# Kernel optimization log

Measured on AMD Instinct MI355X. Metric: run time of the kernel, lower is better.

## Reference

```python
import jax, jax.numpy as jnp
import numpy as np

B, T, D, H = 4, 2048, 1024, 16
HD = D // H  # 64


def setup_inputs() -> dict:
    key = jax.random.key(0)
    ks = jax.random.split(key, 5)
    return {
        "x": jax.random.normal(ks[0], (B, T, D), dtype=jnp.float32),
        "W_qkv": jax.random.normal(ks[1], (D, 3 * D), dtype=jnp.float32) * 0.02,
        "b_qkv": jax.random.normal(ks[2], (3 * D,), dtype=jnp.float32) * 0.02,
        "W_out": jax.random.normal(ks[3], (D, D), dtype=jnp.float32) * 0.02,
        "b_out": jax.random.normal(ks[4], (D,), dtype=jnp.float32) * 0.02,
        "mask": 1,
    }


def reference(x, W_qkv, b_qkv, W_out, b_out, mask):
    # fused QKV projection: (B,T,3D)
    qkv = x @ W_qkv + b_qkv
    # torch layout: view (B,T,H,3*hd) then chunk last dim into q,k,v
    qkv = qkv.reshape(B, T, H, 3, HD)
    q = qkv[..., 0, :].transpose(0, 2, 1, 3)  # (B,H,T,hd)
    k = qkv[..., 1, :].transpose(0, 2, 1, 3)
    v = qkv[..., 2, :].transpose(0, 2, 1, 3)
    scores = jnp.einsum('bhqd,bhkd->bhqk', q, k) / jnp.sqrt(jnp.float32(HD))
    if mask:
        causal = jnp.triu(jnp.ones((T, T), dtype=bool), k=1)
        scores = jnp.where(causal[None, None], jnp.float32(-jnp.inf), scores)
    attn = jax.nn.softmax(scores, axis=-1)
    out = jnp.einsum('bhqk,bhkd->bhqd', attn, v)  # (B,H,T,hd)
    out = out.transpose(0, 2, 1, 3).reshape(B, T, D)
    return out @ W_out + b_out
```

## Files before the change

kernel.cpp:

```cpp
#include <hip/hip_runtime.h>

typedef unsigned short u16;
typedef __bf16 bf16x8 __attribute__((ext_vector_type(8)));
typedef float f32x4 __attribute__((ext_vector_type(4)));
typedef float f32x16 __attribute__((ext_vector_type(16)));

#define DEV __device__ __forceinline__

constexpr int Bb = 4, Tt = 2048, Dd = 1024, Hh = 16, HDd = 64;
constexpr int MM = Bb * Tt;
constexpr float QSCALE = 0.125f * 1.4426950408889634f;

DEV u16 f2bf(float f) {
  unsigned u = __float_as_uint(f);
  u += 0x7fffu + ((u >> 16) & 1u);
  return (u16)(u >> 16);
}

DEV unsigned cvtpk(float a, float b) {
  unsigned r;
  asm("v_cvt_pk_bf16_f32 %0, %1, %2" : "=v"(r) : "v"(a), "v"(b));
  return r;
}

DEV void pswap(unsigned& a, unsigned& b) {
  asm("v_permlane32_swap_b32 %0, %1" : "+v"(a), "+v"(b));
}

DEV void gload_lds16(const u16* g, u16* l) {
  __builtin_amdgcn_global_load_lds(
      (const __attribute__((address_space(1))) void*)g,
      (__attribute__((address_space(3))) void*)l, 16, 0, 0);
}

__global__ __launch_bounds__(256) void cast_x_kernel(const float* __restrict__ in,
                                                     u16* __restrict__ out, int n8) {
  int i = blockIdx.x * 256 + threadIdx.x;
  if (i >= n8) return;
  const float4* p = (const float4*)in + (size_t)i * 2;
  float4 v0 = p[0], v1 = p[1];
  union { u16 u[8]; uint4 v; } t;
  t.u[0] = f2bf(v0.x); t.u[1] = f2bf(v0.y); t.u[2] = f2bf(v0.z); t.u[3] = f2bf(v0.w);
  t.u[4] = f2bf(v1.x); t.u[5] = f2bf(v1.y); t.u[6] = f2bf(v1.z); t.u[7] = f2bf(v1.w);
  ((uint4*)out)[i] = t.v;
}

__global__ __launch_bounds__(256) void wcast_t_kernel(const float* __restrict__ in,
                                                      u16* __restrict__ out, int K, int N) {
  __shared__ float tile[32][33];
  int n0 = blockIdx.x * 32, k0 = blockIdx.y * 32;
  int tx = threadIdx.x & 31, ty = threadIdx.x >> 5;
  #pragma unroll
  for (int yy = ty; yy < 32; yy += 8)
    tile[yy][tx] = in[(size_t)(k0 + yy) * N + n0 + tx];
  __syncthreads();
  #pragma unroll
  for (int yy = ty; yy < 32; yy += 8)
    out[(size_t)(n0 + yy) * K + k0 + tx] = f2bf(tile[tx][yy]);
}

DEV void stageA128(const u16* __restrict__ src, int row0, int k0, int ld, u16* lds) {
  int t = threadIdx.x;
  int r = t >> 2, slot = t & 3;
  int c = (slot ^ ((r >> 1) & 3)) << 3;
  gload_lds16(src + (size_t)(row0 + r) * ld + k0 + c, lds + (size_t)(t & ~63) * 8);
}
DEV void stageB256(const u16* __restrict__ src, int row0, int k0, int ld, u16* lds) {
  int t = threadIdx.x;
  #pragma unroll
  for (int j = 0; j < 2; ++j) {
    int e = j * 512 + t;
    int r = e >> 2, slot = e & 3;
    int c = (slot ^ ((r >> 1) & 3)) << 3;
    gload_lds16(src + (size_t)(row0 + r) * ld + k0 + c,
                lds + (size_t)(j * 512 + (t & ~63)) * 8);
  }
}

__global__ __launch_bounds__(512, 4) void gemm_qkv_kernel(
    const u16* __restrict__ A, const u16* __restrict__ Bt,
    const float* __restrict__ bias,
    u16* __restrict__ Qb, u16* __restrict__ Kb, u16* __restrict__ Vtb,
    int M, int N, int Kd) {
  __shared__ __align__(16) u16 SH[36864];
  int nx = N >> 8;
  int bid = blockIdx.y * nx + blockIdx.x;
  int nwg = (M >> 7) * nx;
  int swz = (bid & 7) * (nwg >> 3) + (bid >> 3);
  int m0 = (swz / nx) * 128, n0 = (swz % nx) * 256;

  int tid = threadIdx.x, l = tid & 63, w = tid >> 6;
  int lo = l & 15, g = l >> 4;
  int wm = (w >> 2) * 64, wn = (w & 3) * 64;
  f32x4 acc[4][4] = {};
  int nk = Kd >> 5;
  stageA128(A, m0, 0, Kd, SH);
  stageB256(Bt, n0, 0, Kd, SH + 12288);
  stageA128(A, m0, 32, Kd, SH + 4096);
  stageB256(Bt, n0, 32, Kd, SH + 12288 + 8192);
  asm volatile("s_waitcnt vmcnt(3)" ::: "memory");
  __builtin_amdgcn_s_barrier();
  for (int kt = 0; kt < nk; ++kt) {
    if (kt + 2 < nk) {
      int bi = (kt + 2) % 3;
      stageA128(A, m0, (kt + 2) * 32, Kd, SH + bi * 4096);
      stageB256(Bt, n0, (kt + 2) * 32, Kd, SH + 12288 + bi * 8192);
    }
    const u16* Ac = SH + (kt % 3) * 4096;
    const u16* Bc = SH + 12288 + (kt % 3) * 8192;
    bf16x8 a[4], b[4];
    #pragma unroll
    for (int i = 0; i < 4; ++i) {
      int row = wm + i * 16 + lo;
      a[i] = *(const bf16x8*)&Ac[row * 32 + ((g ^ ((row >> 1) & 3)) << 3)];
    }
    #pragma unroll
    for (int j = 0; j < 4; ++j) {
      int row = wn + j * 16 + lo;
      b[j] = *(const bf16x8*)&Bc[row * 32 + ((g ^ ((row >> 1) & 3)) << 3)];
    }
    __builtin_amdgcn_s_setprio(1);
    #pragma unroll
    for (int i = 0; i < 4; ++i)
      #pragma unroll
      for (int j = 0; j < 4; ++j)
        acc[i][j] = __builtin_amdgcn_mfma_f32_16x16x32_bf16(a[i], b[j], acc[i][j], 0, 0, 0);
    __builtin_amdgcn_s_setprio(0);
    if (kt + 2 < nk) {
      asm volatile("s_waitcnt vmcnt(3)" ::: "memory");
    } else {
      asm volatile("s_waitcnt vmcnt(0)" ::: "memory");
    }
    __builtin_amdgcn_s_barrier();
  }
  #pragma unroll
  for (int round = 0; round < 2; ++round) {
    if ((w >> 2) == round) {
      u16* ep = SH + (w & 3) * 4096;
      int nblk = n0 + wn;
      int hh = nblk / 192, which = (nblk % 192) >> 6;
      int mblk = m0 + wm;
      int b_ = mblk >> 11, t0 = mblk & (Tt - 1);
      if (which == 2) {
        #pragma unroll
        for (int j = 0; j < 4; ++j) {
          float bv = bias[nblk + j * 16 + lo];
          int rowp = j * 16 + lo;
          #pragma unroll
          for (int i = 0; i < 4; ++i) {
            int slotp = i * 2 + (g >> 1);
            #pragma unroll
            for (int r = 0; r < 4; ++r) {
              ep[rowp * 64 + ((slotp ^ (rowp & 7)) << 3) + (g & 1) * 4 + r] =
                  f2bf(acc[i][j][r] + bv);
            }
          }
        }
        asm volatile("s_waitcnt lgkmcnt(0)" ::: "memory");
        u16* dst = Vtb + (size_t)(b_ * Hh + hh) * HDd * Tt + t0;
        #pragma unroll
        for (int s = 0; s < 8; ++s) {
          int row = s * 8 + (l >> 3);
          int phys = ((l & 7) ^ (row & 7)) << 3;
          uint4 v = *(const uint4*)&ep[row * 64 + phys];
          *(uint4*)(dst + (size_t)row * Tt + (l & 7) * 8) = v;
        }
      } else {
        float qs = (which == 0) ? QSCALE : 1.0f;
        #pragma unroll
        for (int j = 0; j < 4; ++j) {
          float bv = bias[nblk + j * 16 + lo];
          int slot = j * 2 + (lo >> 3);
          #pragma unroll
          for (int i = 0; i < 4; ++i) {
            #pragma unroll
            for (int r = 0; r < 4; ++r) {
              int lrow = i * 16 + g * 4 + r;
              ep[lrow * 64 + ((slot ^ (lrow & 7)) << 3) + (lo & 7)] =
                  f2bf((acc[i][j][r] + bv) * qs);
            }
          }
        }
        asm volatile("s_waitcnt lgkmcnt(0)" ::: "memory");
        u16* dst = (which == 0) ? Qb : Kb;
        dst += ((size_t)(b_ * Hh + hh) * Tt + t0) * HDd;
        #pragma unroll
        for (int s = 0; s < 8; ++s) {
          int row = s * 8 + (l >> 3);
          int phys = ((l & 7) ^ (row & 7)) << 3;
          uint4 v = *(const uint4*)&ep[row * 64 + phys];
          *(uint4*)(dst + row * 64 + (l & 7) * 8) = v;
        }
      }
    }
    __syncthreads();
  }
}

DEV void stage_tile(const u16* __restrict__ src, int row0, int k0, int ld, u16* lds) {
  int t = threadIdx.x, w = t >> 6;
  #pragma unroll
  for (int j = 0; j < 2; ++j) {
    int e = (j * 256 + t) * 8;
    int r = e >> 5;
    int slot = (e >> 3) & 3;
    int c = (slot ^ ((r >> 1) & 3)) << 3;
    gload_lds16(src + (size_t)(row0 + r) * ld + k0 + c, lds + j * 2048 + w * 512);
  }
}

__global__ __launch_bounds__(256) void gemm_out_kernel(
    const u16* __restrict__ A, const u16* __restrict__ Bt,
    const float* __restrict__ bias, float* __restrict__ Cf,
    int M, int N, int Kd) {
  __shared__ __align__(16) u16 SH[24576];
  int nx = N >> 7;
  int bid = blockIdx.y * nx + blockIdx.x;
  int nwg = (M >> 7) * nx;
  int swz = (bid & 7) * (nwg >> 3) + (bid >> 3);
  int m0 = (swz / nx) * 128, n0 = (swz % nx) * 128;

  int tid = threadIdx.x, l = tid & 63, w = tid >> 6;
  int lo = l & 15, g = l >> 4;
  int wm = (w >> 1) * 64, wn = (w & 1) * 64;
  f32x4 acc[4][4] = {};
  int nk = Kd >> 5;
  stage_tile(A, m0, 0, Kd, SH);
  stage_tile(Bt, n0, 0, Kd, SH + 12288);
  stage_tile(A, m0, 32, Kd, SH + 4096);
  stage_tile(Bt, n0, 32, Kd, SH + 12288 + 4096);
  asm volatile("s_waitcnt vmcnt(4)" ::: "memory");
  __builtin_amdgcn_s_barrier();
  for (int kt = 0; kt < nk; ++kt) {
    if (kt + 2 < nk) {
      int bi = (kt + 2) % 3;
      stage_tile(A, m0, (kt + 2) * 32, Kd, SH + bi * 4096);
      stage_tile(Bt, n0, (kt + 2) * 32, Kd, SH + 12288 + bi * 4096);
    }
    const u16* Ac = SH + (kt % 3) * 4096;
    const u16* Bc = SH + 12288 + (kt % 3) * 4096;
    bf16x8 a[4], b[4];
    #pragma unroll
    for (int i = 0; i < 4; ++i) {
      int row = wm + i * 16 + lo;
      a[i] = *(const bf16x8*)&Ac[row * 32 + ((g ^ ((row >> 1) & 3)) << 3)];
    }
    #pragma unroll
    for (int j = 0; j < 4; ++j) {
      int row = wn + j * 16 + lo;
      b[j] = *(const bf16x8*)&Bc[row * 32 + ((g ^ ((row >> 1) & 3)) << 3)];
    }
    #pragma unroll
    for (int i = 0; i < 4; ++i)
      #pragma unroll
      for (int j = 0; j < 4; ++j)
        acc[i][j] = __builtin_amdgcn_mfma_f32_16x16x32_bf16(a[i], b[j], acc[i][j], 0, 0, 0);
    if (kt + 2 < nk) {
      asm volatile("s_waitcnt vmcnt(4)" ::: "memory");
    } else {
      asm volatile("s_waitcnt vmcnt(0)" ::: "memory");
    }
    __builtin_amdgcn_s_barrier();
  }
  #pragma unroll
  for (int j = 0; j < 4; ++j) {
    int n = n0 + wn + j * 16 + lo;
    float bv = bias[n];
    #pragma unroll
    for (int i = 0; i < 4; ++i) {
      #pragma unroll
      for (int r = 0; r < 4; ++r) {
        int m = m0 + wm + i * 16 + g * 4 + r;
        Cf[(size_t)m * N + n] = acc[i][j][r] + bv;
      }
    }
  }
}

DEV void stage512(const u16* __restrict__ g, size_t rstride, u16* lds) {
  int t = threadIdx.x;
  int r = t >> 3, pp = t & 7;
  int lg = pp ^ (r & 7);
  gload_lds16(g + (size_t)r * rstride + lg * 8, lds + (size_t)(t & ~63) * 8);
}

DEV void build_pfrags(const f32x16& s, bf16x8& f0, bf16x8& f1) {
  unsigned w0 = cvtpk(s[0], s[1]),  w1 = cvtpk(s[2], s[3]);
  unsigned w2 = cvtpk(s[4], s[5]),  w3 = cvtpk(s[6], s[7]);
  unsigned w4 = cvtpk(s[8], s[9]),  w5 = cvtpk(s[10], s[11]);
  unsigned w6 = cvtpk(s[12], s[13]), w7 = cvtpk(s[14], s[15]);
  pswap(w0, w2);
  pswap(w1, w3);
  pswap(w4, w6);
  pswap(w5, w7);
  union { unsigned u[4]; bf16x8 v; } t0, t1;
  t0.u[0] = w0; t0.u[1] = w1; t0.u[2] = w2; t0.u[3] = w3;
  t1.u[0] = w4; t1.u[1] = w5; t1.u[2] = w6; t1.u[3] = w7;
  f0 = t0.v; f1 = t1.v;
}

DEV void write_o(u16* __restrict__ O, size_t rowbase, const f32x16& o0,
                 const f32x16& o1, float L, int hf) {
  float inv = 1.0f / L;
  #pragma unroll
  for (int m = 0; m < 4; ++m) {
    uint2 v0, v1;
    v0.x = cvtpk(o0[4 * m] * inv,     o0[4 * m + 1] * inv);
    v0.y = cvtpk(o0[4 * m + 2] * inv, o0[4 * m + 3] * inv);
    *(uint2*)(O + rowbase + m * 8 + hf * 4) = v0;
    v1.x = cvtpk(o1[4 * m] * inv,     o1[4 * m + 1] * inv);
    v1.y = cvtpk(o1[4 * m + 2] * inv, o1[4 * m + 3] * inv);
    *(uint2*)(O + rowbase + 32 + m * 8 + hf * 4) = v1;
  }
}

__global__ __launch_bounds__(512) void attn_kernel(const u16* __restrict__ Q,
                                                   const u16* __restrict__ K,
                                                   const u16* __restrict__ Vt,
                                                   u16* __restrict__ O) {
  __shared__ __align__(16) u16 Ks[4][4096];
  __shared__ __align__(16) u16 Vs[4][4096];
  __shared__ float MLs[8][64][2];
  __shared__ float OSs[4][64][8];
  int p = blockIdx.y & 7;
  int bh = ((int)blockIdx.y >> 3) * 8 + (int)blockIdx.x;
  int b_ = bh >> 4, h = bh & 15;
  const u16* Qp = Q + (size_t)bh * Tt * HDd;
  const u16* Kp = K + (size_t)bh * Tt * HDd;
  const u16* Vp = Vt + (size_t)bh * HDd * Tt;
  int tid = threadIdx.x, w = tid >> 6, l = tid & 63;
  int wq = w & 3, grp = w >> 2;
  int lq = l & 31, hf = l >> 5;
  int JA = 15 - p, JB = p;
  int ntA = 2 * JA + 2;
  constexpr int ntT = 34;

  int q0 = 128 * JA + 32 * wq;
  int qrow = q0 + lq;
  int swz = lq & 7;

  bf16x8 aq[4];
  #pragma unroll
  for (int s = 0; s < 4; ++s)
    aq[s] = *(const bf16x8*)(Qp + (size_t)qrow * HDd + s * 16 + hf * 8);

  f32x16 o0 = {}, o1 = {};
  float M = -1e30f, L = 0.f;

  stage512(Kp, HDd, Ks[0]);
  stage512(Vp, Tt, Vs[0]);
  stage512(Kp + (size_t)64 * HDd, HDd, Ks[1]);
  stage512(Vp + 64, Tt, Vs[1]);
  asm volatile("s_waitcnt vmcnt(0)" ::: "memory");
  __builtin_amdgcn_s_barrier();

  int jB = ntA >> 1;
  for (int j = 0; j < ntT / 2; ++j) {
    int t2 = 2 * j + 2;
    if (t2 < ntT) {
      int kt2 = (t2 < ntA ? t2 : t2 - ntA) * 64;
      stage512(Kp + (size_t)kt2 * HDd, HDd, Ks[t2 & 3]);
      stage512(Vp + kt2, Tt, Vs[t2 & 3]);
      int t3 = t2 + 1;
      int kt3 = (t3 < ntA ? t3 : t3 - ntA) * 64;
      stage512(Kp + (size_t)kt3 * HDd, HDd, Ks[t3 & 3]);
      stage512(Vp + kt3, Tt, Vs[t3 & 3]);
    }
    if (j == jB) {
      MLs[w][l][0] = M; MLs[w][l][1] = L;
      asm volatile("s_waitcnt lgkmcnt(0)" ::: "memory");
      __builtin_amdgcn_s_barrier();
      float Mb = MLs[w ^ 4][l][0], Lb = MLs[w ^ 4][l][1];
      float Mstar = fmaxf(M, Mb);
      float ss = __builtin_amdgcn_exp2f(M - Mstar);
      float sb = __builtin_amdgcn_exp2f(Mb - Mstar);
      float Lm = L * ss + Lb * sb;
      #pragma unroll
      for (int r = 0; r < 16; ++r) { o0[r] *= ss; o1[r] *= ss; }
      #pragma unroll
      for (int c = 0; c < 4; ++c) {
        if (w >= 4) {
          #pragma unroll
          for (int k = 0; k < 8; ++k)
            OSs[wq][l][k] = (c < 2) ? o0[(c & 1) * 8 + k] : o1[(c & 1) * 8 + k];
        }
        asm volatile("s_waitcnt lgkmcnt(0)" ::: "memory");
        __builtin_amdgcn_s_barrier();
        if (w < 4) {
          #pragma unroll
          for (int k = 0; k < 8; ++k) {
            float v = OSs[wq][l][k];
            if (c < 2) o0[(c & 1) * 8 + k] += v; else o1[(c & 1) * 8 + k] += v;
          }
        }
        asm volatile("s_waitcnt lgkmcnt(0)" ::: "memory");
        __builtin_amdgcn_s_barrier();
      }
      if (w < 4) {
        size_t rbA = ((size_t)b_ * Tt + qrow) * Dd + h * HDd;
        write_o(O, rbA, o0, o1, Lm, hf);
      }
      #pragma unroll
      for (int r = 0; r < 16; ++r) { o0[r] = 0.f; o1[r] = 0.f; }
      M = -1e30f; L = 0.f;
      q0 = 128 * JB + 32 * wq;
      qrow = q0 + lq;
      #pragma unroll
      for (int s = 0; s < 4; ++s)
        aq[s] = *(const bf16x8*)(Qp + (size_t)qrow * HDd + s * 16 + hf * 8);
    }
    int myt = 2 * j + grp;
    int kt = (myt < ntA ? myt : myt - ntA) * 64;
    const u16* Kc = Ks[myt & 3];
    const u16* Vc = Vs[myt & 3];
    if (kt < q0 + 32) {
      f32x16 s0 = {}, s1 = {};
      __builtin_amdgcn_s_setprio(1);
      #pragma unroll
      for (int ds = 0; ds < 4; ++ds) {
        int slot = 2 * ds + hf;
        bf16x8 k0 = *(const bf16x8*)&Kc[lq * 64 + ((slot ^ swz) << 3)];
        bf16x8 k1 = *(const bf16x8*)&Kc[(32 + lq) * 64 + ((slot ^ swz) << 3)];
        s0 = __builtin_amdgcn_mfma_f32_32x32x16_bf16(k0, aq[ds], s0, 0, 0, 0);
        s1 = __builtin_amdgcn_mfma_f32_32x32x16_bf16(k1, aq[ds], s1, 0, 0, 0);
      }
      __builtin_amdgcn_s_setprio(0);
      if (kt + 63 > q0) {
        #pragma unroll
        for (int r = 0; r < 16; ++r) {
          int kg = kt + (r & 3) + 8 * (r >> 2) + 4 * hf;
          if (kg > qrow)      s0[r] = -INFINITY;
          if (kg + 32 > qrow) s1[r] = -INFINITY;
        }
      }
      float mx_[16];
      #pragma unroll
      for (int r = 0; r < 16; ++r) mx_[r] = fmaxf(s0[r], s1[r]);
      #pragma unroll
      for (int st = 8; st >= 1; st >>= 1)
        #pragma unroll
        for (int r = 0; r < 16; ++r) if (r < st) mx_[r] = fmaxf(mx_[r], mx_[r + st]);
      float mx = fmaxf(mx_[0], __shfl_xor(mx_[0], 32));
      float sc = 1.f;
      if (!__all(mx <= M + 8.f)) {
        float Mn = fmaxf(M, mx);
        sc = __builtin_amdgcn_exp2f(M - Mn);
        M = Mn;
        #pragma unroll
        for (int r = 0; r < 16; ++r) { o0[r] *= sc; o1[r] *= sc; }
      }
      #pragma unroll
      for (int r = 0; r < 16; ++r) {
        s0[r] = __builtin_amdgcn_exp2f(s0[r] - M);
        s1[r] = __builtin_amdgcn_exp2f(s1[r] - M);
      }
      float ls_[16];
      #pragma unroll
      for (int r = 0; r < 16; ++r) ls_[r] = s0[r] + s1[r];
      #pragma unroll
      for (int st = 8; st >= 1; st >>= 1)
        #pragma unroll
        for (int r = 0; r < 16; ++r) if (r < st) ls_[r] += ls_[r + st];
      float ls = ls_[0] + __shfl_xor(ls_[0], 32);
      L = L * sc + ls;
      bf16x8 pf0, pf1, pf2, pf3;
      build_pfrags(s0, pf0, pf1);
      build_pfrags(s1, pf2, pf3);
      __builtin_amdgcn_s_setprio(1);
      #pragma unroll
      for (int ks = 0; ks < 4; ++ks) {
        int slot = 2 * ks + hf;
        bf16x8 v0 = *(const bf16x8*)&Vc[lq * 64 + ((slot ^ swz) << 3)];
        bf16x8 v1 = *(const bf16x8*)&Vc[(32 + lq) * 64 + ((slot ^ swz) << 3)];
        bf16x8 pf = (ks == 0) ? pf0 : (ks == 1) ? pf1 : (ks == 2) ? pf2 : pf3;
        o0 = __builtin_amdgcn_mfma_f32_32x32x16_bf16(v0, pf, o0, 0, 0, 0);
        o1 = __builtin_amdgcn_mfma_f32_32x32x16_bf16(v1, pf, o1, 0, 0, 0);
      }
      __builtin_amdgcn_s_setprio(0);
    }
    asm volatile("s_waitcnt vmcnt(0)" ::: "memory");
    __builtin_amdgcn_s_barrier();
  }

  MLs[w][l][0] = M; MLs[w][l][1] = L;
  asm volatile("s_waitcnt lgkmcnt(0)" ::: "memory");
  __builtin_amdgcn_s_barrier();
  float Mb = MLs[w ^ 4][l][0], Lb = MLs[w ^ 4][l][1];
  float Mstar = fmaxf(M, Mb);
  float ss = __builtin_amdgcn_exp2f(M - Mstar);
  float sb = __builtin_amdgcn_exp2f(Mb - Mstar);
  float Lm = L * ss + Lb * sb;
  #pragma unroll
  for (int r = 0; r < 16; ++r) { o0[r] *= ss; o1[r] *= ss; }
  #pragma unroll
  for (int c = 0; c < 4; ++c) {
    if (w >= 4) {
      #pragma unroll
      for (int k = 0; k < 8; ++k)
        OSs[wq][l][k] = (c < 2) ? o0[(c & 1) * 8 + k] : o1[(c & 1) * 8 + k];
    }
    asm volatile("s_waitcnt lgkmcnt(0)" ::: "memory");
    __builtin_amdgcn_s_barrier();
    if (w < 4) {
      #pragma unroll
      for (int k = 0; k < 8; ++k) {
        float v = OSs[wq][l][k];
        if (c < 2) o0[(c & 1) * 8 + k] += v; else o1[(c & 1) * 8 + k] += v;
      }
    }
    asm volatile("s_waitcnt lgkmcnt(0)" ::: "memory");
    __builtin_amdgcn_s_barrier();
  }
  if (w < 4) {
    size_t rbB = ((size_t)b_ * Tt + qrow) * Dd + h * HDd;
    write_o(O, rbB, o0, o1, Lm, hf);
  }
}

extern "C" void kernel_launch(void* const* d_in, const int* in_sizes, int n_in,
                              void* d_out, int out_size, void* d_ws, size_t ws_size,
                              hipStream_t stream) {
  const float* x    = (const float*)d_in[0];
  const float* Wqkv = (const float*)d_in[1];
  const float* bqkv = (const float*)d_in[2];
  const float* Wout = (const float*)d_in[3];
  const float* bout = (const float*)d_in[4];
  float* out = (float*)d_out;
  char* ws = (char*)d_ws;

  u16* xb    = (u16*)(ws + 0);
  u16* Ob    = (u16*)(ws + 0);
  u16* Wqkvt = (u16*)(ws + 16777216);
  u16* Woutt = (u16*)(ws + 23068672);
  u16* Qb    = (u16*)(ws + 25165824);
  u16* Kb    = (u16*)(ws + 41943040);
  u16* Vtb   = (u16*)(ws + 58720256);

  cast_x_kernel<<<4096, 256, 0, stream>>>(x, xb, (MM * Dd) / 8);
  wcast_t_kernel<<<dim3(96, 32), 256, 0, stream>>>(Wqkv, Wqkvt, Dd, 3 * Dd);
  wcast_t_kernel<<<dim3(32, 32), 256, 0, stream>>>(Wout, Woutt, Dd, Dd);
  gemm_qkv_kernel<<<dim3(12, 64), 512, 0, stream>>>(
      xb, Wqkvt, bqkv, Qb, Kb, Vtb, MM, 3 * Dd, Dd);
  attn_kernel<<<dim3(8, 64), 512, 0, stream>>>(Qb, Kb, Vtb, Ob);
  gemm_out_kernel<<<dim3(8, 64), 256, 0, stream>>>(
      Ob, Woutt, bout, out, MM, Dd, Dd);
}
```

Before: 172.4 us.

## Widen output GEMM to 128x256 tiles and split attention merge into smaller chunks

The output projection GEMM now uses 128x256 tiles with 512 threads (8 waves) instead of 128x128 with 256 threads. It reuses stageA128/stageB256 helpers that appear to exist elsewhere, and raises wave priority around the MFMA block. This is meant to improve reuse of the A operand and cut the number of workgroups, at the cost of more LDS per block. Separately, the attention kernel's cross-wave output merge now moves 4 floats per step over 8 barrier rounds instead of 8 floats over 4, which halves that LDS scratch but adds barriers.

```diff
diff --git a/kernel.cpp b/kernel.cpp
--- a/kernel.cpp
+++ b/kernel.cpp
@@ -197,48 +197,36 @@
   }
 }
 
-DEV void stage_tile(const u16* __restrict__ src, int row0, int k0, int ld, u16* lds) {
-  int t = threadIdx.x, w = t >> 6;
-  #pragma unroll
-  for (int j = 0; j < 2; ++j) {
-    int e = (j * 256 + t) * 8;
-    int r = e >> 5;
-    int slot = (e >> 3) & 3;
-    int c = (slot ^ ((r >> 1) & 3)) << 3;
-    gload_lds16(src + (size_t)(row0 + r) * ld + k0 + c, lds + j * 2048 + w * 512);
-  }
-}
-
-__global__ __launch_bounds__(256) void gemm_out_kernel(
+__global__ __launch_bounds__(512, 4) void gemm_out256_kernel(
     const u16* __restrict__ A, const u16* __restrict__ Bt,
     const float* __restrict__ bias, float* __restrict__ Cf,
     int M, int N, int Kd) {
-  __shared__ __align__(16) u16 SH[24576];
-  int nx = N >> 7;
+  __shared__ __align__(16) u16 SH[36864];
+  int nx = N >> 8;
   int bid = blockIdx.y * nx + blockIdx.x;
   int nwg = (M >> 7) * nx;
   int swz = (bid & 7) * (nwg >> 3) + (bid >> 3);
-  int m0 = (swz / nx) * 128, n0 = (swz % nx) * 128;
+  int m0 = (swz / nx) * 128, n0 = (swz % nx) * 256;
 
   int tid = threadIdx.x, l = tid & 63, w = tid >> 6;
   int lo = l & 15, g = l >> 4;
-  int wm = (w >> 1) * 64, wn = (w & 1) * 64;
+  int wm = (w >> 2) * 64, wn = (w & 3) * 64;
   f32x4 acc[4][4] = {};
   int nk = Kd >> 5;
-  stage_tile(A, m0, 0, Kd, SH);
-  stage_tile(Bt, n0, 0, Kd, SH + 12288);
-  stage_tile(A, m0, 32, Kd, SH + 4096);
-  stage_tile(Bt, n0, 32, Kd, SH + 12288 + 4096);
-  asm volatile("s_waitcnt vmcnt(4)" ::: "memory");
+  stageA128(A, m0, 0, Kd, SH);
+  stageB256(Bt, n0, 0, Kd, SH + 12288);
+  stageA128(A, m0, 32, Kd, SH + 4096);
+  stageB256(Bt, n0, 32, Kd, SH + 12288 + 8192);
+  asm volatile("s_waitcnt vmcnt(3)" ::: "memory");
   __builtin_amdgcn_s_barrier();
   for (int kt = 0; kt < nk; ++kt) {
     if (kt + 2 < nk) {
       int bi = (kt + 2) % 3;
-      stage_tile(A, m0, (kt + 2) * 32, Kd, SH + bi * 4096);
-      stage_tile(Bt, n0, (kt + 2) * 32, Kd, SH + 12288 + bi * 4096);
+      stageA128(A, m0, (kt + 2) * 32, Kd, SH + bi * 4096);
+      stageB256(Bt, n0, (kt + 2) * 32, Kd, SH + 12288 + bi * 8192);
     }
     const u16* Ac = SH + (kt % 3) * 4096;
-    const u16* Bc = SH + 12288 + (kt % 3) * 4096;
+    const u16* Bc = SH + 12288 + (kt % 3) * 8192;
     bf16x8 a[4], b[4];
     #pragma unroll
     for (int i = 0; i < 4; ++i) {
@@ -250,13 +238,15 @@
       int row = wn + j * 16 + lo;
       b[j] = *(const bf16x8*)&Bc[row * 32 + ((g ^ ((row >> 1) & 3)) << 3)];
     }
+    __builtin_amdgcn_s_setprio(1);
     #pragma unroll
     for (int i = 0; i < 4; ++i)
       #pragma unroll
       for (int j = 0; j < 4; ++j)
         acc[i][j] = __builtin_amdgcn_mfma_f32_16x16x32_bf16(a[i], b[j], acc[i][j], 0, 0, 0);
+    __builtin_amdgcn_s_setprio(0);
     if (kt + 2 < nk) {
-      asm volatile("s_waitcnt vmcnt(4)" ::: "memory");
+      asm volatile("s_waitcnt vmcnt(3)" ::: "memory");
     } else {
       asm volatile("s_waitcnt vmcnt(0)" ::: "memory");
     }
@@ -321,7 +311,7 @@
   __shared__ __align__(16) u16 Ks[4][4096];
   __shared__ __align__(16) u16 Vs[4][4096];
   __shared__ float MLs[8][64][2];
-  __shared__ float OSs[4][64][8];
+  __shared__ float OSs[4][64][4];
   int p = blockIdx.y & 7;
   int bh = ((int)blockIdx.y >> 3) * 8 + (int)blockIdx.x;
   int b_ = bh >> 4, h = bh & 15;
@@ -378,19 +368,19 @@
       #pragma unroll
       for (int r = 0; r < 16; ++r) { o0[r] *= ss; o1[r] *= ss; }
       #pragma unroll
-      for (int c = 0; c < 4; ++c) {
+      for (int c = 0; c < 8; ++c) {
         if (w >= 4) {
           #pragma unroll
-          for (int k = 0; k < 8; ++k)
-            OSs[wq][l][k] = (c < 2) ? o0[(c & 1) * 8 + k] : o1[(c & 1) * 8 + k];
+          for (int k = 0; k < 4; ++k)
+            OSs[wq][l][k] = (c < 4) ? o0[c * 4 + k] : o1[(c - 4) * 4 + k];
         }
         asm volatile("s_waitcnt lgkmcnt(0)" ::: "memory");
         __builtin_amdgcn_s_barrier();
         if (w < 4) {
           #pragma unroll
-          for (int k = 0; k < 8; ++k) {
+          for (int k = 0; k < 4; ++k) {
             float v = OSs[wq][l][k];
-            if (c < 2) o0[(c & 1) * 8 + k] += v; else o1[(c & 1) * 8 + k] += v;
+            if (c < 4) o0[c * 4 + k] += v; else o1[(c - 4) * 4 + k] += v;
           }
         }
         asm volatile("s_waitcnt lgkmcnt(0)" ::: "memory");
@@ -493,19 +483,19 @@
   #pragma unroll
   for (int r = 0; r < 16; ++r) { o0[r] *= ss; o1[r] *= ss; }
   #pragma unroll
-  for (int c = 0; c < 4; ++c) {
+  for (int c = 0; c < 8; ++c) {
     if (w >= 4) {
       #pragma unroll
-      for (int k = 0; k < 8; ++k)
-        OSs[wq][l][k] = (c < 2) ? o0[(c & 1) * 8 + k] : o1[(c & 1) * 8 + k];
+      for (int k = 0; k < 4; ++k)
+        OSs[wq][l][k] = (c < 4) ? o0[c * 4 + k] : o1[(c - 4) * 4 + k];
     }
     asm volatile("s_waitcnt lgkmcnt(0)" ::: "memory");
     __builtin_amdgcn_s_barrier();
     if (w < 4) {
       #pragma unroll
-      for (int k = 0; k < 8; ++k) {
+      for (int k = 0; k < 4; ++k) {
         float v = OSs[wq][l][k];
-        if (c < 2) o0[(c & 1) * 8 + k] += v; else o1[(c & 1) * 8 + k] += v;
+        if (c < 4) o0[c * 4 + k] += v; else o1[(c - 4) * 4 + k] += v;
       }
     }
     asm volatile("s_waitcnt lgkmcnt(0)" ::: "memory");
@@ -542,6 +532,6 @@
   gemm_qkv_kernel<<<dim3(12, 64), 512, 0, stream>>>(
       xb, Wqkvt, bqkv, Qb, Kb, Vtb, MM, 3 * Dd, Dd);
   attn_kernel<<<dim3(8, 64), 512, 0, stream>>>(Qb, Kb, Vtb, Ob);
-  gemm_out_kernel<<<dim3(8, 64), 256, 0, stream>>>(
+  gemm_out256_kernel<<<dim3(4, 64), 512, 0, stream>>>(
       Ob, Woutt, bout, out, MM, Dd, Dd);
 }
```

After: 174.6 us (median of 2 runs). No clear change (+1.2%).

## Rework QKV GEMM to 4 waves with 64x128 warp tiles; widen out-proj tile

Applied to the files above, without the earlier changes.

The QKV projection GEMM now runs with 256 threads, so each wave computes a 64x128 output tile (32 MFMA accumulators) instead of 64x64. The staging helpers are adapted to 256 threads and the epilogue is run per wave over two 64-column head blocks, with no cross-wave rounds. The output-projection GEMM switches to a 512-thread, 128x256-tile kernel derived from the old QKV kernel, giving a 4x64 grid. The larger per-wave tiles raise register pressure and lower occupancy in exchange for more reuse of the A/B fragments read from LDS.

```diff
diff --git a/kernel.cpp b/kernel.cpp
--- a/kernel.cpp
+++ b/kernel.cpp
@@ -77,10 +77,151 @@
   }
 }
 
-__global__ __launch_bounds__(512, 4) void gemm_qkv_kernel(
+DEV void stageA128_t256(const u16* __restrict__ src, int row0, int k0, int ld, u16* lds) {
+  int t = threadIdx.x;
+  #pragma unroll
+  for (int j = 0; j < 2; ++j) {
+    int e = j * 256 + t;
+    int r = e >> 2, slot = e & 3;
+    int c = (slot ^ ((r >> 1) & 3)) << 3;
+    gload_lds16(src + (size_t)(row0 + r) * ld + k0 + c,
+                lds + (size_t)(j * 256 + (t & ~63)) * 8);
+  }
+}
+DEV void stageB256_t256(const u16* __restrict__ src, int row0, int k0, int ld, u16* lds) {
+  int t = threadIdx.x;
+  #pragma unroll
+  for (int j = 0; j < 4; ++j) {
+    int e = j * 256 + t;
+    int r = e >> 2, slot = e & 3;
+    int c = (slot ^ ((r >> 1) & 3)) << 3;
+    gload_lds16(src + (size_t)(row0 + r) * ld + k0 + c,
+                lds + (size_t)(j * 256 + (t & ~63)) * 8);
+  }
+}
+
+__global__ __launch_bounds__(256, 2) void gemm_qkv_kernel(
     const u16* __restrict__ A, const u16* __restrict__ Bt,
     const float* __restrict__ bias,
     u16* __restrict__ Qb, u16* __restrict__ Kb, u16* __restrict__ Vtb,
+    int M, int N, int Kd) {
+  __shared__ __align__(16) u16 SH[36864];
+  int nx = N >> 8;
+  int bid = blockIdx.y * nx + blockIdx.x;
+  int nwg = (M >> 7) * nx;
+  int swz = (bid & 7) * (nwg >> 3) + (bid >> 3);
+  int m0 = (swz / nx) * 128, n0 = (swz % nx) * 256;
+
+  int tid = threadIdx.x, l = tid & 63, w = tid >> 6;
+  int lo = l & 15, g = l >> 4;
+  int wm = (w >> 1) * 64, wn = (w & 1) * 128;
+  f32x4 acc[4][8] = {};
+  int nk = Kd >> 5;
+  stageA128_t256(A, m0, 0, Kd, SH);
+  stageB256_t256(Bt, n0, 0, Kd, SH + 12288);
+  stageA128_t256(A, m0, 32, Kd, SH + 4096);
+  stageB256_t256(Bt, n0, 32, Kd, SH + 12288 + 8192);
+  asm volatile("s_waitcnt vmcnt(6)" ::: "memory");
+  __builtin_amdgcn_s_barrier();
+  for (int kt = 0; kt < nk; ++kt) {
+    if (kt + 2 < nk) {
+      int bi = (kt + 2) % 3;
+      stageA128_t256(A, m0, (kt + 2) * 32, Kd, SH + bi * 4096);
+      stageB256_t256(Bt, n0, (kt + 2) * 32, Kd, SH + 12288 + bi * 8192);
+    }
+    const u16* Ac = SH + (kt % 3) * 4096;
+    const u16* Bc = SH + 12288 + (kt % 3) * 8192;
+    bf16x8 a[4], b[8];
+    #pragma unroll
+    for (int i = 0; i < 4; ++i) {
+      int row = wm + i * 16 + lo;
+      a[i] = *(const bf16x8*)&Ac[row * 32 + ((g ^ ((row >> 1) & 3)) << 3)];
+    }
+    #pragma unroll
+    for (int j = 0; j < 8; ++j) {
+      int row = wn + j * 16 + lo;
+      b[j] = *(const bf16x8*)&Bc[row * 32 + ((g ^ ((row >> 1) & 3)) << 3)];
+    }
+    __builtin_amdgcn_s_setprio(1);
+    #pragma unroll
+    for (int i = 0; i < 4; ++i)
+      #pragma unroll
+      for (int j = 0; j < 8; ++j)
+        acc[i][j] = __builtin_amdgcn_mfma_f32_16x16x32_bf16(a[i], b[j], acc[i][j], 0, 0, 0);
+    __builtin_amdgcn_s_setprio(0);
+    if (kt + 2 < nk) {
+      asm volatile("s_waitcnt vmcnt(6)" ::: "memory");
+    } else {
+      asm volatile("s_waitcnt vmcnt(0)" ::: "memory");
+    }
+    __builtin_amdgcn_s_barrier();
+  }
+  u16* ep = SH + w * 4096;
+  int mblk = m0 + wm;
+  int b_ = mblk >> 11, t0 = mblk & (Tt - 1);
+  #pragma unroll
+  for (int cb = 0; cb < 2; ++cb) {
+    int nblk = n0 + wn + cb * 64;
+    int hh = nblk / 192, which = (nblk % 192) >> 6;
+    if (which == 2) {
+      #pragma unroll
+      for (int j = 0; j < 4; ++j) {
+        float bv = bias[nblk + j * 16 + lo];
+        int rowp = j * 16 + lo;
+        #pragma unroll
+        for (int i = 0; i < 4; ++i) {
+          int slotp = i * 2 + (g >> 1);
+          #pragma unroll
+          for (int r = 0; r < 4; ++r) {
+            ep[rowp * 64 + ((slotp ^ (rowp & 7)) << 3) + (g & 1) * 4 + r] =
+                f2bf(acc[i][cb * 4 + j][r] + bv);
+          }
+        }
+      }
+      asm volatile("s_waitcnt lgkmcnt(0)" ::: "memory");
+      u16* dst = Vtb + (size_t)(b_ * Hh + hh) * HDd * Tt + t0;
+      #pragma unroll
+      for (int s = 0; s < 8; ++s) {
+        int row = s * 8 + (l >> 3);
+        int phys = ((l & 7) ^ (row & 7)) << 3;
+        uint4 v = *(const uint4*)&ep[row * 64 + phys];
+        *(uint4*)(dst + (size_t)row * Tt + (l & 7) * 8) = v;
+      }
+      asm volatile("s_waitcnt lgkmcnt(0)" ::: "memory");
+    } else {
+      float qs = (which == 0) ? QSCALE : 1.0f;
+      #pragma unroll
+      for (int j = 0; j < 4; ++j) {
+        float bv = bias[nblk + j * 16 + lo];
+        int slot = j * 2 + (lo >> 3);
+        #pragma unroll
+        for (int i = 0; i < 4; ++i) {
+          #pragma unroll
+          for (int r = 0; r < 4; ++r) {
+            int lrow = i * 16 + g * 4 + r;
+            ep[lrow * 64 + ((slot ^ (lrow & 7)) << 3) + (lo & 7)] =
+                f2bf((acc[i][cb * 4 + j][r] + bv) * qs);
+          }
+        }
+      }
+      asm volatile("s_waitcnt lgkmcnt(0)" ::: "memory");
+      u16* dst = (which == 0) ? Qb : Kb;
+      dst += ((size_t)(b_ * Hh + hh) * Tt + t0) * HDd;
+      #pragma unroll
+      for (int s = 0; s < 8; ++s) {
+        int row = s * 8 + (l >> 3);
+        int phys = ((l & 7) ^ (row & 7)) << 3;
+        uint4 v = *(const uint4*)&ep[row * 64 + phys];
+        *(uint4*)(dst + row * 64 + (l & 7) * 8) = v;
+      }
+      asm volatile("s_waitcnt lgkmcnt(0)" ::: "memory");
+    }
+  }
+}
+
+__global__ __launch_bounds__(512, 4) void gemm_out256_kernel(
+    const u16* __restrict__ A, const u16* __restrict__ Bt,
+    const float* __restrict__ bias, float* __restrict__ Cf,
     int M, int N, int Kd) {
   __shared__ __align__(16) u16 SH[36864];
   int nx = N >> 8;
@@ -128,135 +269,6 @@
     __builtin_amdgcn_s_setprio(0);
     if (kt + 2 < nk) {
       asm volatile("s_waitcnt vmcnt(3)" ::: "memory");
-    } else {
-      asm volatile("s_waitcnt vmcnt(0)" ::: "memory");
-    }
-    __builtin_amdgcn_s_barrier();
-  }
-  #pragma unroll
-  for (int round = 0; round < 2; ++round) {
-    if ((w >> 2) == round) {
-      u16* ep = SH + (w & 3) * 4096;
-      int nblk = n0 + wn;
-      int hh = nblk / 192, which = (nblk % 192) >> 6;
-      int mblk = m0 + wm;
-      int b_ = mblk >> 11, t0 = mblk & (Tt - 1);
-      if (which == 2) {
-        #pragma unroll
-        for (int j = 0; j < 4; ++j) {
-          float bv = bias[nblk + j * 16 + lo];
-          int rowp = j * 16 + lo;
-          #pragma unroll
-          for (int i = 0; i < 4; ++i) {
-            int slotp = i * 2 + (g >> 1);
-            #pragma unroll
-            for (int r = 0; r < 4; ++r) {
-              ep[rowp * 64 + ((slotp ^ (rowp & 7)) << 3) + (g & 1) * 4 + r] =
-                  f2bf(acc[i][j][r] + bv);
-            }
-          }
-        }
-        asm volatile("s_waitcnt lgkmcnt(0)" ::: "memory");
-        u16* dst = Vtb + (size_t)(b_ * Hh + hh) * HDd * Tt + t0;
-        #pragma unroll
-        for (int s = 0; s < 8; ++s) {
-          int row = s * 8 + (l >> 3);
-          int phys = ((l & 7) ^ (row & 7)) << 3;
-          uint4 v = *(const uint4*)&ep[row * 64 + phys];
-          *(uint4*)(dst + (size_t)row * Tt + (l & 7) * 8) = v;
-        }
-      } else {
-        float qs = (which == 0) ? QSCALE : 1.0f;
-        #pragma unroll
-        for (int j = 0; j < 4; ++j) {
-          float bv = bias[nblk + j * 16 + lo];
-          int slot = j * 2 + (lo >> 3);
-          #pragma unroll
-          for (int i = 0; i < 4; ++i) {
-            #pragma unroll
-            for (int r = 0; r < 4; ++r) {
-              int lrow = i * 16 + g * 4 + r;
-              ep[lrow * 64 + ((slot ^ (lrow & 7)) << 3) + (lo & 7)] =
-                  f2bf((acc[i][j][r] + bv) * qs);
-            }
-          }
-        }
-        asm volatile("s_waitcnt lgkmcnt(0)" ::: "memory");
-        u16* dst = (which == 0) ? Qb : Kb;
-        dst += ((size_t)(b_ * Hh + hh) * Tt + t0) * HDd;
-        #pragma unroll
-        for (int s = 0; s < 8; ++s) {
-          int row = s * 8 + (l >> 3);
-          int phys = ((l & 7) ^ (row & 7)) << 3;
-          uint4 v = *(const uint4*)&ep[row * 64 + phys];
-          *(uint4*)(dst + row * 64 + (l & 7) * 8) = v;
-        }
-      }
-    }
-    __syncthreads();
-  }
-}
-
-DEV void stage_tile(const u16* __restrict__ src, int row0, int k0, int ld, u16* lds) {
-  int t = threadIdx.x, w = t >> 6;
-  #pragma unroll
-  for (int j = 0; j < 2; ++j) {
-    int e = (j * 256 + t) * 8;
-    int r = e >> 5;
-    int slot = (e >> 3) & 3;
-    int c = (slot ^ ((r >> 1) & 3)) << 3;
-    gload_lds16(src + (size_t)(row0 + r) * ld + k0 + c, lds + j * 2048 + w * 512);
-  }
-}
-
-__global__ __launch_bounds__(256) void gemm_out_kernel(
-    const u16* __restrict__ A, const u16* __restrict__ Bt,
-    const float* __restrict__ bias, float* __restrict__ Cf,
-    int M, int N, int Kd) {
-  __shared__ __align__(16) u16 SH[24576];
-  int nx = N >> 7;
-  int bid = blockIdx.y * nx + blockIdx.x;
-  int nwg = (M >> 7) * nx;
-  int swz = (bid & 7) * (nwg >> 3) + (bid >> 3);
-  int m0 = (swz / nx) * 128, n0 = (swz % nx) * 128;
-
-  int tid = threadIdx.x, l = tid & 63, w = tid >> 6;
-  int lo = l & 15, g = l >> 4;
-  int wm = (w >> 1) * 64, wn = (w & 1) * 64;
-  f32x4 acc[4][4] = {};
-  int nk = Kd >> 5;
-  stage_tile(A, m0, 0, Kd, SH);
-  stage_tile(Bt, n0, 0, Kd, SH + 12288);
-  stage_tile(A, m0, 32, Kd, SH + 4096);
-  stage_tile(Bt, n0, 32, Kd, SH + 12288 + 4096);
-  asm volatile("s_waitcnt vmcnt(4)" ::: "memory");
-  __builtin_amdgcn_s_barrier();
-  for (int kt = 0; kt < nk; ++kt) {
-    if (kt + 2 < nk) {
-      int bi = (kt + 2) % 3;
-      stage_tile(A, m0, (kt + 2) * 32, Kd, SH + bi * 4096);
-      stage_tile(Bt, n0, (kt + 2) * 32, Kd, SH + 12288 + bi * 4096);
-    }
-    const u16* Ac = SH + (kt % 3) * 4096;
-    const u16* Bc = SH + 12288 + (kt % 3) * 4096;
-    bf16x8 a[4], b[4];
-    #pragma unroll
-    for (int i = 0; i < 4; ++i) {
-      int row = wm + i * 16 + lo;
-      a[i] = *(const bf16x8*)&Ac[row * 32 + ((g ^ ((row >> 1) & 3)) << 3)];
-    }
-    #pragma unroll
-    for (int j = 0; j < 4; ++j) {
-      int row = wn + j * 16 + lo;
-      b[j] = *(const bf16x8*)&Bc[row * 32 + ((g ^ ((row >> 1) & 3)) << 3)];
-    }
-    #pragma unroll
-    for (int i = 0; i < 4; ++i)
-      #pragma unroll
-      for (int j = 0; j < 4; ++j)
-        acc[i][j] = __builtin_amdgcn_mfma_f32_16x16x32_bf16(a[i], b[j], acc[i][j], 0, 0, 0);
-    if (kt + 2 < nk) {
-      asm volatile("s_waitcnt vmcnt(4)" ::: "memory");
     } else {
       asm volatile("s_waitcnt vmcnt(0)" ::: "memory");
     }
@@ -539,9 +551,9 @@
   cast_x_kernel<<<4096, 256, 0, stream>>>(x, xb, (MM * Dd) / 8);
   wcast_t_kernel<<<dim3(96, 32), 256, 0, stream>>>(Wqkv, Wqkvt, Dd, 3 * Dd);
   wcast_t_kernel<<<dim3(32, 32), 256, 0, stream>>>(Wout, Woutt, Dd, Dd);
-  gemm_qkv_kernel<<<dim3(12, 64), 512, 0, stream>>>(
+  gemm_qkv_kernel<<<dim3(12, 64), 256, 0, stream>>>(
       xb, Wqkvt, bqkv, Qb, Kb, Vtb, MM, 3 * Dd, Dd);
   attn_kernel<<<dim3(8, 64), 512, 0, stream>>>(Qb, Kb, Vtb, Ob);
-  gemm_out_kernel<<<dim3(8, 64), 256, 0, stream>>>(
+  gemm_out256_kernel<<<dim3(4, 64), 512, 0, stream>>>(
       Ob, Woutt, bout, out, MM, Dd, Dd);
 }
```

Result: no change. 174.1 us (+0.9%).
